# Performance work log

Hardware: AMD Instinct MI355X
Metric: run time of the kernel (lower is better)

The kernel has to match this reference:

```python
import jax, jax.numpy as jnp
import numpy as np

B, S, DIM = 4, 2048, 2048
H, KVH, HD = 32, 8, 64
REPEATS = H // KVH
SCALE = HD ** -0.5


def _rope(x, cos, sin):
    # x: (B, S, Hn, HD); cos/sin: (S, HD//2)
    xr = x[..., 0::2]
    xi = x[..., 1::2]
    c = cos[:, None, :]  # (S, 1, HD//2) broadcasts over heads
    s = sin[:, None, :]
    out_r = xr * c - xi * s
    out_i = xr * s + xi * c
    return jnp.stack([out_r, out_i], axis=-1).reshape(x.shape)


def setup_inputs() -> dict:
    key = jax.random.key(0)
    ks = jax.random.split(key, 5)
    x = jax.random.normal(ks[0], (B, S, DIM), dtype=jnp.float32)
    wq = jax.random.normal(ks[1], (H * HD, DIM), dtype=jnp.float32) * 0.02
    wk = jax.random.normal(ks[2], (KVH * HD, DIM), dtype=jnp.float32) * 0.02
    wv = jax.random.normal(ks[3], (KVH * HD, DIM), dtype=jnp.float32) * 0.02
    wo = jax.random.normal(ks[4], (DIM, H * HD), dtype=jnp.float32) * 0.02
    # standard RoPE frequencies: freqs_cis = exp(i * t * theta)
    inv_freq = 1.0 / (10000.0 ** (jnp.arange(0, HD, 2, dtype=jnp.float32) / HD))
    angles = jnp.arange(S, dtype=jnp.float32)[:, None] * inv_freq[None, :]  # (S, HD//2)
    return {
        "x": x, "wq": wq, "wk": wk, "wv": wv, "wo": wo,
        "freqs_cos": jnp.cos(angles), "freqs_sin": jnp.sin(angles),
    }


def reference(x, wq, wk, wv, wo, freqs_cos, freqs_sin):
    b, s, _ = x.shape
    q = (x @ wq.T).reshape(b, s, H, HD)
    k = (x @ wk.T).reshape(b, s, KVH, HD)
    v = (x @ wv.T).reshape(b, s, KVH, HD)
    q = _rope(q, freqs_cos, freqs_sin)
    k = _rope(k, freqs_cos, freqs_sin)
    k_rep = jnp.repeat(k, REPEATS, axis=2)  # (B,S,H,HD)
    v_rep = jnp.repeat(v, REPEATS, axis=2)
    # NOTE: faithful to source - q is NOT transposed to (B,H,S,HD), so the
    # matmul contracts head_dim at each token, producing (B,S,H,H) scores
    # (mixing across heads per position), softmaxed over the last head axis.
    scores = jnp.einsum('bshd,bsed->bshe', q, k_rep) * SCALE  # (B,S,H,H)
    weights = jax.nn.softmax(scores, axis=-1)
    out = jnp.einsum('bshe,bsed->bshd', weights, v_rep)  # (B,S,H,HD)
    out = out.reshape(b, s, H * HD)
    return out @ wo.T
```

## Files before the change

kernel.cpp:

```cpp
#include <hip/hip_runtime.h>

typedef unsigned short u16;
typedef __bf16 bf16x8 __attribute__((ext_vector_type(8)));
typedef float f32x4 __attribute__((ext_vector_type(4)));

#define AS1 __attribute__((address_space(1)))
#define AS3 __attribute__((address_space(3)))

__device__ inline u16 f2bf(float f) {
    union { float f; unsigned u; } c; c.f = f;
    unsigned u = c.u;
    u += 0x7fffu + ((u >> 16) & 1u);
    return (u16)(u >> 16);
}
__device__ inline float bf2f(u16 b) {
    union { unsigned u; float f; } c; c.u = ((unsigned)b) << 16;
    return c.f;
}

__device__ inline void async_cp16(const void* g, void* l) {
    __builtin_amdgcn_global_load_lds((const AS1 void*)g, (AS3 void*)l, 16, 0, 0);
}

__global__ __launch_bounds__(256)
void conv_all(const float* __restrict__ x,
              const float* __restrict__ wq, const float* __restrict__ wk,
              const float* __restrict__ wv, const float* __restrict__ wo,
              u16* __restrict__ x_bf, u16* __restrict__ wqkv,
              u16* __restrict__ wo_bf) {
    int b = blockIdx.x;
    if (b < 8192) {
        int i = (b * 256 + threadIdx.x) * 8;
        float4 f0 = *(const float4*)(x + i);
        float4 f1 = *(const float4*)(x + i + 4);
        union { u16 h[8]; uint4 v; } o;
        o.h[0] = f2bf(f0.x); o.h[1] = f2bf(f0.y);
        o.h[2] = f2bf(f0.z); o.h[3] = f2bf(f0.w);
        o.h[4] = f2bf(f1.x); o.h[5] = f2bf(f1.y);
        o.h[6] = f2bf(f1.z); o.h[7] = f2bf(f1.w);
        *(uint4*)(x_bf + i) = o.v;
    } else {
        int i = ((b - 8192) * 256 + threadIdx.x) * 4;
        const float* src;
        u16* dst;
        if (i < 4194304)       { src = wq + i;           dst = wqkv + i; }
        else if (i < 5242880)  { src = wk + (i-4194304); dst = wqkv + i; }
        else if (i < 6291456)  { src = wv + (i-5242880); dst = wqkv + i; }
        else                   { src = wo + (i-6291456); dst = wo_bf + (i-6291456); }
        float4 f = *(const float4*)src;
        union { u16 h[4]; uint2 v; } o;
        o.h[0] = f2bf(f.x); o.h[1] = f2bf(f.y);
        o.h[2] = f2bf(f.z); o.h[3] = f2bf(f.w);
        *(uint2*)dst = o.v;
    }
}

template <int NI, bool BF16_OUT>
__global__ __launch_bounds__(512, 2)
void gemm_bt8(const u16* __restrict__ A, const u16* __restrict__ B,
              void* __restrict__ Cout, int N, int K) {
    constexpr int SZ = 32768 + NI * 8192;
    __shared__ __align__(16) char ldsc[2 * SZ];

    const int tid  = threadIdx.x;
    const int w    = tid >> 6;
    const int lane = tid & 63;
    const int row0 = blockIdx.x * 256;
    const int col0 = blockIdx.y * (NI * 64);
    const int wm = w >> 2, wn = w & 3;
    const int lm = lane & 15, quad = lane >> 4;

    const int NT  = K / 64;
    const int NIT = K / 128;
    const int K64 = K * 64;

    const int sr  = lane >> 3;
    const int stC = ((lane & 7) ^ sr) * 8;
    const u16* pA = A + (size_t)(row0 + w * 8 + sr) * K + stC;
    const u16* pB = B + (size_t)(col0 + w * 8 + sr) * K + stC;
    const int stagoff = w * 1024;

    const int cx0   = (quad ^ (lm & 7)) * 16;
    const int cx1   = cx0 ^ 64;
    const int aBase = (wm * 128 + lm) * 128;
    const int bBase = 32768 + (wn * (NI * 16) + lm) * 128;

    f32x4 acc[8][NI];
#pragma unroll
    for (int i = 0; i < 8; i++)
#pragma unroll
        for (int j = 0; j < NI; j++) acc[i][j] = (f32x4){0.f, 0.f, 0.f, 0.f};

    auto stage = [&](const u16* base, int v, int unit, int regionOff) {
        int kb = (v < NT ? v : NT - 1) * 64;
        async_cp16(base + (size_t)unit * K64 + kb,
                   ldsc + (v & 1) * SZ + regionOff + unit * 8192 + stagoff);
    };
#define ST_A(v, u) stage(pA, (v), (u), 0)
#define ST_B(v, u) stage(pB, (v), (u), 32768)

#define LDR(off) (*(const bf16x8*)(ldsc + (off)))
#define SB __builtin_amdgcn_sched_barrier(0)
#define BAR __builtin_amdgcn_s_barrier()
#define WLG(n) asm volatile("s_waitcnt lgkmcnt(" #n ")" ::: "memory")

#define RD_AF(DST, BASEOFF, MIBASE)                                           \
    _Pragma("unroll")                                                         \
    for (int j = 0; j < 2; j++) {                                             \
        DST[j][0] = LDR((BASEOFF) + aBase + ((MIBASE) + j) * 2048 + cx0);     \
        DST[j][1] = LDR((BASEOFF) + aBase + ((MIBASE) + j) * 2048 + cx1);     \
    }
#define RD_BG(DST, BASEOFF)                                                   \
    _Pragma("unroll")                                                         \
    for (int ni = 0; ni < NI; ni++) {                                         \
        DST[ni][0] = LDR((BASEOFF) + bBase + ni * 2048 + cx0);                \
        DST[ni][1] = LDR((BASEOFF) + bBase + ni * 2048 + cx1);                \
    }
#define MFMA_TAIL(MI0, AF, BG)                                                \
    __builtin_amdgcn_s_setprio(1);                                            \
    _Pragma("unroll")                                                         \
    for (int s = 0; s < 2; s++)                                               \
        _Pragma("unroll")                                                     \
        for (int j = 0; j < 2; j++)                                           \
            _Pragma("unroll")                                                 \
            for (int ni = 0; ni < NI; ni++)                                   \
                acc[(MI0) + j][ni] = __builtin_amdgcn_mfma_f32_16x16x32_bf16( \
                    AF[j][s], BG[ni][s], acc[(MI0) + j][ni], 0, 0, 0);        \
    __builtin_amdgcn_s_setprio(0);

    bf16x8 bgA[NI][2], bgB[NI][2], F[2][2], G[2][2];

#pragma unroll
    for (int u = 0; u < 4; u++) ST_A(0, u);
#pragma unroll
    for (int u = 0; u < NI; u++) ST_B(0, u);
#pragma unroll
    for (int u = 0; u < NI; u++) ST_B(1, u);
    ST_A(1, 0);
    if constexpr (NI == 3) asm volatile("s_waitcnt vmcnt(4)" ::: "memory");
    else                   asm volatile("s_waitcnt vmcnt(5)" ::: "memory");
    SB;
    if constexpr (NI == 3) { RD_BG(bgA, 0) }
    RD_AF(F, 0, 0)
    SB;
    BAR;

#define HALF_ITER(u, BO, BN, BGC, BGN)                                        \
    {                                                                         \
                                                                      \
        if constexpr (NI == 4) { RD_BG(BGC, BO) }                             \
        SB;                                                                   \
        RD_AF(G, BO, 2)                                                       \
        SB;                                                                   \
        ST_A((u) + 1, 1); ST_A((u) + 1, 2); ST_A((u) + 1, 3);                 \
        SB;                                                                   \
        BAR;                                                                  \
        WLG(4);                                                               \
        SB;                                                                   \
        MFMA_TAIL(0, F, BGC)                                                  \
        SB;                                                                   \
        BAR;                                                                  \
                                                                      \
        RD_AF(F, BO, 4)                                                       \
        SB;                                                                   \
        ST_B((u) + 2, 0); ST_B((u) + 2, 1);                                   \
        SB;                                                                   \
        BAR;                                                                  \
        WLG(4);                                                               \
        SB;                                                                   \
        MFMA_TAIL(2, G, BGC)                                                  \
        SB;                                                                   \
        BAR;                                                                  \
                                                                      \
        RD_AF(G, BO, 6)                                                       \
        SB;                                                                   \
        ST_B((u) + 2, 2);                                                     \
        if constexpr (NI == 4) { ST_B((u) + 2, 3); }                          \
        ST_A((u) + 2, 0);                                                     \
        SB;                                                                   \
        BAR;                                                                  \
        WLG(4);                                                               \
        SB;                                                                   \
        MFMA_TAIL(4, F, BGC)                                                  \
        SB;                                                                   \
        BAR;                                                                  \
                               \
        WLG(0);                                                               \
        SB;                                                                   \
        MFMA_TAIL(6, G, BGC)                                                  \
        SB;                                                                   \
        if constexpr (NI == 3) asm volatile("s_waitcnt vmcnt(4)" ::: "memory");\
        else                   asm volatile("s_waitcnt vmcnt(5)" ::: "memory");\
        SB;                                                                   \
        if constexpr (NI == 3) { RD_BG(BGN, BN) }                             \
        RD_AF(F, BN, 0)                                                       \
        SB;                                                                   \
        BAR;                                                                  \
    }

    for (int it = 0; it < NIT; ++it) {
        const int t = 2 * it;
        HALF_ITER(t, 0, SZ, bgA, bgB)
        HALF_ITER(t + 1, SZ, 0, bgB, bgA)
    }

#undef HALF_ITER
#undef MFMA_TAIL
#undef RD_BG
#undef RD_AF
#undef WLG
#undef BAR
#undef SB
#undef LDR
#undef ST_A
#undef ST_B

    const int rbase = row0 + wm * 128 + quad * 4;
    const int cbase = col0 + wn * (NI * 16) + lm;
    if (BF16_OUT) {
        u16* C = (u16*)Cout;
#pragma unroll
        for (int mi = 0; mi < 8; mi++)
#pragma unroll
            for (int r = 0; r < 4; r++) {
                size_t ro = (size_t)(rbase + mi * 16 + r) * N;
#pragma unroll
                for (int ni = 0; ni < NI; ni++)
                    C[ro + cbase + ni * 16] = f2bf(acc[mi][ni][r]);
            }
    } else {
        float* C = (float*)Cout;
#pragma unroll
        for (int mi = 0; mi < 8; mi++)
#pragma unroll
            for (int r = 0; r < 4; r++) {
                size_t ro = (size_t)(rbase + mi * 16 + r) * N;
#pragma unroll
                for (int ni = 0; ni < NI; ni++)
                    C[ro + cbase + ni * 16] = acc[mi][ni][r];
            }
    }
}

__global__ __launch_bounds__(256)
void attn_tok(const u16* __restrict__ qkv, u16* __restrict__ out) {
    __shared__ float kvf[1024];
    const int tok = blockIdx.x;
    const int t = threadIdx.x;
    const u16* qrow = qkv + (size_t)tok * 3072;

    {
        uint2 w = *(const uint2*)(qrow + 2048 + t * 4);
        kvf[t * 4 + 0] = bf2f((u16)(w.x & 0xffff));
        kvf[t * 4 + 1] = bf2f((u16)(w.x >> 16));
        kvf[t * 4 + 2] = bf2f((u16)(w.y & 0xffff));
        kvf[t * 4 + 3] = bf2f((u16)(w.y >> 16));
    }
    __syncthreads();

    const int h = t >> 3, j = t & 7;
    float qf[8];
    {
        uint4 w = *(const uint4*)(qrow + h * 64 + j * 8);
        unsigned ws4[4] = {w.x, w.y, w.z, w.w};
#pragma unroll
        for (int i = 0; i < 4; i++) {
            qf[2 * i]     = bf2f((u16)(ws4[i] & 0xffff));
            qf[2 * i + 1] = bf2f((u16)(ws4[i] >> 16));
        }
    }

    float s[8];
#pragma unroll
    for (int g = 0; g < 8; g++) {
        const float* kk = kvf + g * 64 + j * 8;
        float a = 0.f;
#pragma unroll
        for (int d = 0; d < 8; d++) a += qf[d] * kk[d];
        s[g] = a;
    }
#pragma unroll
    for (int g = 0; g < 8; g++) {
        s[g] += __shfl_xor(s[g], 1);
        s[g] += __shfl_xor(s[g], 2);
        s[g] += __shfl_xor(s[g], 4);
    }
    float m = -1e30f;
#pragma unroll
    for (int g = 0; g < 8; g++) { s[g] *= 0.125f; m = fmaxf(m, s[g]); }
    float p[8], l = 0.f;
#pragma unroll
    for (int g = 0; g < 8; g++) { p[g] = __expf(s[g] - m); l += p[g]; }
    float rl = 1.f / l;

    float o[8] = {0, 0, 0, 0, 0, 0, 0, 0};
#pragma unroll
    for (int g = 0; g < 8; g++) {
        float w = p[g] * rl;
        const float* vv = kvf + 512 + g * 64 + j * 8;
#pragma unroll
        for (int d = 0; d < 8; d++) o[d] += w * vv[d];
    }

    unsigned po[4];
#pragma unroll
    for (int i = 0; i < 4; i++)
        po[i] = (unsigned)f2bf(o[2 * i]) | ((unsigned)f2bf(o[2 * i + 1]) << 16);
    uint4 wo_; wo_.x = po[0]; wo_.y = po[1]; wo_.z = po[2]; wo_.w = po[3];
    *(uint4*)(out + (size_t)tok * 2048 + h * 64 + j * 8) = wo_;
}

extern "C" void kernel_launch(void* const* d_in, const int* in_sizes, int n_in,
                              void* d_out, int out_size, void* d_ws, size_t ws_size,
                              hipStream_t stream) {
    const float* x  = (const float*)d_in[0];
    const float* wq = (const float*)d_in[1];
    const float* wk = (const float*)d_in[2];
    const float* wv = (const float*)d_in[3];
    const float* wo = (const float*)d_in[4];

    u16* x_bf  = (u16*)d_ws;
    u16* wqkv  = x_bf  + 16777216;
    u16* wo_bf = wqkv  + 6291456;
    u16* qkv   = wo_bf + 4194304;
    u16* attn  = x_bf;

    conv_all<<<18432, dim3(256), 0, stream>>>(x, wq, wk, wv, wo, x_bf, wqkv, wo_bf);

    gemm_bt8<3, true><<<dim3(32, 16), dim3(512), 0, stream>>>(x_bf, wqkv, qkv,
                                                              3072, 2048);

    attn_tok<<<8192, dim3(256), 0, stream>>>(qkv, attn);

    gemm_bt8<4, false><<<dim3(32, 8), dim3(512), 0, stream>>>(attn, wo_bf,
                                                              (float*)d_out,
                                                              2048, 2048);
}
```

Before: 319.2 us.

## Add GEMM variant streaming B operand directly from global into registers

Adds a new GEMM kernel for the QKV projection in which only the A tile is staged through LDS, loaded into registers and then written to a double buffer. The B fragments are read straight from global memory into registers and prefetched one k-step ahead. The main loop is finely scheduled with sched barriers, explicit waitcnts and setprio around the MFMA groups. The goal is to cut LDS capacity and bandwidth pressure for B and to overlap global loads with compute. The cost is more register pressure and uncoalesced or redundant global reads of B across waves.

```diff
diff --git a/kernel.cpp b/kernel.cpp
--- a/kernel.cpp
+++ b/kernel.cpp
@@ -3,6 +3,7 @@
 typedef unsigned short u16;
 typedef __bf16 bf16x8 __attribute__((ext_vector_type(8)));
 typedef float f32x4 __attribute__((ext_vector_type(4)));
+typedef unsigned int u32x4 __attribute__((ext_vector_type(4)));
 
 #define AS1 __attribute__((address_space(1)))
 #define AS3 __attribute__((address_space(3)))
@@ -57,6 +58,185 @@
 
 template <int NI, bool BF16_OUT>
 __global__ __launch_bounds__(512, 2)
+void gemm_breg(const u16* __restrict__ A, const u16* __restrict__ B,
+               void* __restrict__ Cout, int N, int K) {
+    __shared__ __align__(16) char ldsc[65536];
+
+    const int tid  = threadIdx.x;
+    const int w    = tid >> 6;
+    const int lane = tid & 63;
+    const int row0 = blockIdx.x * 256;
+    const int col0 = blockIdx.y * (NI * 64);
+    const int wm = w >> 2, wn = w & 3;
+    const int lm = lane & 15, quad = lane >> 4;
+
+    const int NT  = K / 64;
+    const int NIT = K / 128;
+    const int K64 = K * 64;
+
+    const int sr  = lane >> 3;
+    const int stC = ((lane & 7) ^ sr) * 8;
+    const u16* pA = A + (size_t)(row0 + w * 8 + sr) * K + stC;
+    const int wrOff = w * 1024 + lane * 16;
+
+    const int cx0   = (quad ^ (lm & 7)) * 16;
+    const int cx1   = cx0 ^ 64;
+    const int aBase = (wm * 128 + lm) * 128;
+
+    const u16* pB = B + (size_t)(col0 + wn * (NI * 16) + lm) * K + quad * 8;
+
+    f32x4 acc[8][NI];
+#pragma unroll
+    for (int i = 0; i < 8; i++)
+#pragma unroll
+        for (int j = 0; j < NI; j++) acc[i][j] = (f32x4){0.f, 0.f, 0.f, 0.f};
+
+#define LDRB(off) (*(const bf16x8*)(ldsc + (off)))
+#define SBq __builtin_amdgcn_sched_barrier(0)
+#define BARq __builtin_amdgcn_s_barrier()
+#define WLGq(n) asm volatile("s_waitcnt lgkmcnt(" #n ")" ::: "memory")
+
+#define LD_AREG(V)                                                            \
+    {                                                                         \
+        int kb_ = ((V) < NT ? (V) : NT - 1) * 64;      \
+        _Pragma("unroll")                                                     \
+        for (int uu = 0; uu < 4; uu++)                                        \
+            areg[uu] = *(const AS1 u32x4*)(pA + (size_t)uu * K64 + kb_);      \
+    }
+#define WR_AREG(BUF)                                                          \
+    _Pragma("unroll")                                                         \
+    for (int uu = 0; uu < 4; uu++)                                            \
+        *(u32x4*)(ldsc + (BUF) + uu * 8192 + wrOff) = areg[uu];
+#define RD_A2(DST, BASEOFF, MIBASE)                                           \
+    _Pragma("unroll")                                                         \
+    for (int j = 0; j < 2; j++) {                                             \
+        DST[j][0] = LDRB((BASEOFF) + aBase + ((MIBASE) + j) * 2048 + cx0);    \
+        DST[j][1] = LDRB((BASEOFF) + aBase + ((MIBASE) + j) * 2048 + cx1);    \
+    }
+#define LD_BG(DST, V)                                                         \
+    {                                                                         \
+        int kb_ = ((V) < NT ? (V) : NT - 1) * 64;                             \
+        _Pragma("unroll")                                                     \
+        for (int ni = 0; ni < NI; ni++) {                                     \
+            DST[ni][0] = *(const AS1 bf16x8*)(pB + (size_t)ni * 16 * K + kb_);\
+            DST[ni][1] = *(const AS1 bf16x8*)(pB + (size_t)ni * 16 * K + kb_ + 32);\
+        }                                                                     \
+    }
+#define MFMA_T(MI0, AF, BG)                                                   \
+    __builtin_amdgcn_s_setprio(1);                                            \
+    _Pragma("unroll")                                                         \
+    for (int s = 0; s < 2; s++)                                               \
+        _Pragma("unroll")                                                     \
+        for (int j = 0; j < 2; j++)                                           \
+            _Pragma("unroll")                                                 \
+            for (int ni = 0; ni < NI; ni++)                                   \
+                acc[(MI0) + j][ni] = __builtin_amdgcn_mfma_f32_16x16x32_bf16( \
+                    AF[j][s], BG[ni][s], acc[(MI0) + j][ni], 0, 0, 0);        \
+    __builtin_amdgcn_s_setprio(0);
+
+    bf16x8 bgA[NI][2], bgB[NI][2], F[2][2], G[2][2];
+    u32x4 areg[4];
+
+    LD_AREG(0)
+    SBq;
+    LD_BG(bgA, 0)
+    SBq;
+    WR_AREG(0)
+    SBq;
+    WLGq(0);
+    BARq;
+
+#define HALF_B(u, BO, BN, BGC, BGN)                                           \
+    {                                                                         \
+                    \
+        RD_A2(F, BO, 0)                                                       \
+        SBq;                                                                  \
+        RD_A2(G, BO, 2)                                                       \
+        SBq;                                                                  \
+        LD_AREG((u) + 1)                                                      \
+        SBq;                                                                  \
+        BARq;                                                                 \
+        WLGq(4);                                                              \
+        SBq;                                                                  \
+        MFMA_T(0, F, BGC)                                                     \
+        SBq;                                                                  \
+        BARq;                                                                 \
+                              \
+        RD_A2(F, BO, 4)                                                       \
+        SBq;                                                                  \
+        LD_BG(BGN, (u) + 1)                                                   \
+        SBq;                                                                  \
+        BARq;                                                                 \
+        WLGq(4);                                                              \
+        SBq;                                                                  \
+        MFMA_T(2, G, BGC)                                                     \
+        SBq;                                                                  \
+        BARq;                                                                 \
+                                                      \
+        RD_A2(G, BO, 6)                                                       \
+        SBq;                                                                  \
+        BARq;                                                                 \
+        WLGq(4);                                                              \
+        SBq;                                                                  \
+        MFMA_T(4, F, BGC)                                                     \
+        SBq;                                                                  \
+        BARq;                                                                 \
+            \
+        WR_AREG(BN)                                                           \
+        SBq;                                                                  \
+        WLGq(0);                                                              \
+        SBq;                                                                  \
+        MFMA_T(6, G, BGC)                                                     \
+        SBq;                                                                  \
+        BARq;                                                                 \
+    }
+
+    for (int it = 0; it < NIT; ++it) {
+        const int t = 2 * it;
+        HALF_B(t, 0, 32768, bgA, bgB)
+        HALF_B(t + 1, 32768, 0, bgB, bgA)
+    }
+
+#undef HALF_B
+#undef MFMA_T
+#undef LD_BG
+#undef RD_A2
+#undef WR_AREG
+#undef LD_AREG
+#undef WLGq
+#undef BARq
+#undef SBq
+#undef LDRB
+
+    const int rbase = row0 + wm * 128 + quad * 4;
+    const int cbase = col0 + wn * (NI * 16) + lm;
+    if (BF16_OUT) {
+        u16* C = (u16*)Cout;
+#pragma unroll
+        for (int mi = 0; mi < 8; mi++)
+#pragma unroll
+            for (int r = 0; r < 4; r++) {
+                size_t ro = (size_t)(rbase + mi * 16 + r) * N;
+#pragma unroll
+                for (int ni = 0; ni < NI; ni++)
+                    C[ro + cbase + ni * 16] = f2bf(acc[mi][ni][r]);
+            }
+    } else {
+        float* C = (float*)Cout;
+#pragma unroll
+        for (int mi = 0; mi < 8; mi++)
+#pragma unroll
+            for (int r = 0; r < 4; r++) {
+                size_t ro = (size_t)(rbase + mi * 16 + r) * N;
+#pragma unroll
+                for (int ni = 0; ni < NI; ni++)
+                    C[ro + cbase + ni * 16] = acc[mi][ni][r];
+            }
+    }
+}
+
+template <int NI, bool BF16_OUT>
+__global__ __launch_bounds__(512, 2)
 void gemm_bt8(const u16* __restrict__ A, const u16* __restrict__ B,
               void* __restrict__ Cout, int N, int K) {
     constexpr int SZ = 32768 + NI * 8192;
@@ -327,8 +507,8 @@
 
     conv_all<<<18432, dim3(256), 0, stream>>>(x, wq, wk, wv, wo, x_bf, wqkv, wo_bf);
 
-    gemm_bt8<3, true><<<dim3(32, 16), dim3(512), 0, stream>>>(x_bf, wqkv, qkv,
-                                                              3072, 2048);
+    gemm_breg<3, true><<<dim3(32, 16), dim3(512), 0, stream>>>(x_bf, wqkv, qkv,
+                                                               3072, 2048);
 
     attn_tok<<<8192, dim3(256), 0, stream>>>(qkv, attn);
 
```

Result: slower. 362.1 us (+13.4%).
